# Kernel tuning notes

Hardware: AMD Instinct MI355X
Metric: run time of the kernel (lower is better)

Reference implementation:

```python
import jax, jax.numpy as jnp
import numpy as np

N, E = 50000, 800000
D_IN, D_DEG, D_H, D_UP = 96, 32, 256, 128
EPS = 0.0  # non-trainable buffer, initial_eps=0


def setup_inputs() -> dict:
    key = jax.random.key(0)
    ks = jax.random.split(key, 8)
    d = D_IN + D_DEG  # 128, feature dim after degree-as-tag concat
    return {
        "x": jax.random.normal(ks[0], (N, D_IN), dtype=jnp.float32),
        "degrees": jax.random.uniform(ks[1], (N, D_DEG), dtype=jnp.float32),
        "edge_features": jax.random.normal(ks[2], (E, d), dtype=jnp.float32),
        "W1": jax.random.normal(ks[3], (d, D_H), dtype=jnp.float32) * (1.0 / np.sqrt(d)),
        "b1": jnp.zeros((D_H,), dtype=jnp.float32),
        "W2": jax.random.normal(ks[4], (D_H, D_UP), dtype=jnp.float32) * (1.0 / np.sqrt(D_H)),
        "b2": jnp.zeros((D_UP,), dtype=jnp.float32),
        "edge_index": jax.random.randint(ks[5], (2, E), 0, N, dtype=jnp.int64),
    }


def reference(x, degrees, edge_features, W1, b1, W2, b2, edge_index):
    # degree_as_tag + retain_features: concat node features with degree tags
    h = jnp.concatenate([x, degrees], axis=-1)  # [N, 128]
    # flow='source_to_target': source j = edge_index[0], target i = edge_index[1]
    src, dst = edge_index[0], edge_index[1]
    msgs = jax.nn.relu(h[src] + edge_features)  # [E, 128]
    agg = jax.ops.segment_sum(msgs, dst, num_segments=N)  # [N, 128]
    z = (1.0 + EPS) * h + agg
    # update MLP: Linear -> ReLU -> Linear
    out = jax.nn.relu(z @ W1 + b1) @ W2 + b2  # [N, 128]
    return out
```

## Files before the change

### kernel.cpp

```cpp
#include <hip/hip_runtime.h>


constexpr int DIN  = 96;
constexpr int DDEG = 32;
constexpr int D    = 128;
constexpr int DH   = 256;
constexpr int DUP  = 128;

typedef short bf16x8 __attribute__((ext_vector_type(8)));
typedef float f32x4  __attribute__((ext_vector_type(4)));

static __device__ __forceinline__ ushort f2bf(float f) {
    unsigned u = __float_as_uint(f);
    unsigned r = (u + 0x7fff + ((u >> 16) & 1)) >> 16;
    return (ushort)r;
}
static __device__ __forceinline__ float4 bf4_to_f4(ushort4 u) {
    float4 r;
    r.x = __uint_as_float((unsigned)u.x << 16);
    r.y = __uint_as_float((unsigned)u.y << 16);
    r.z = __uint_as_float((unsigned)u.z << 16);
    r.w = __uint_as_float((unsigned)u.w << 16);
    return r;
}

static __device__ __forceinline__ int waveInclScan(int v, int lane) {
#pragma unroll
    for (int off = 1; off < 64; off <<= 1) {
        int t = __shfl_up(v, off, 64);
        if (lane >= off) v += t;
    }
    return v;
}

__global__ __launch_bounds__(256) void init_h_kernel(
    const float* __restrict__ x, const float* __restrict__ deg,
    ushort* __restrict__ hp, int N) {
    int t = blockIdx.x * 256 + threadIdx.x;
    if (t >= N * 32) return;
    int n = t >> 5, c = t & 31;
    float4 v;
    if (c < 24) v = *reinterpret_cast<const float4*>(&x[(size_t)n * DIN + c * 4]);
    else        v = *reinterpret_cast<const float4*>(&deg[(size_t)n * DDEG + (c - 24) * 4]);
    ushort4 o;
    o.x = f2bf(v.x); o.y = f2bf(v.y); o.z = f2bf(v.z); o.w = f2bf(v.w);
    *reinterpret_cast<ushort4*>(&hp[(size_t)n * D + c * 4]) = o;
}

__global__ __launch_bounds__(256) void count_kernel(
    const int* __restrict__ ei, int* __restrict__ counts, int N, int E) {
    int e = blockIdx.x * 256 + threadIdx.x;
    if (e >= E) return;
    atomicAdd(&counts[ei[E + e]], 1);
}

__global__ __launch_bounds__(256) void scan_partial_kernel(
    const int* __restrict__ counts, int* __restrict__ blockSums, int N) {
    const int tid = threadIdx.x;
    int base = blockIdx.x * 1024 + tid * 4;
    int4 c = make_int4(0, 0, 0, 0);
    if (base + 3 < N) c = *reinterpret_cast<const int4*>(&counts[base]);
    else if (base < N) {
        c.x = counts[base];
        if (base + 1 < N) c.y = counts[base + 1];
        if (base + 2 < N) c.z = counts[base + 2];
    }
    int s = c.x + c.y + c.z + c.w;
#pragma unroll
    for (int off = 32; off; off >>= 1) s += __shfl_xor(s, off, 64);
    __shared__ int wsum[4];
    if ((tid & 63) == 0) wsum[tid >> 6] = s;
    __syncthreads();
    if (tid == 0) blockSums[blockIdx.x] = wsum[0] + wsum[1] + wsum[2] + wsum[3];
}

__global__ __launch_bounds__(64) void scan_base_kernel(
    const int* __restrict__ blockSums, int* __restrict__ blockBase, int nb) {
    int l = threadIdx.x;
    int orig = (l < nb) ? blockSums[l] : 0;
    int incl = waveInclScan(orig, l);
    if (l < nb) blockBase[l] = incl - orig;
}

__global__ __launch_bounds__(256) void scan_final_kernel(
    const int* __restrict__ counts, const int* __restrict__ blockBase,
    int* __restrict__ offsets, int* __restrict__ cursor, int N, int E) {
    const int tid = threadIdx.x, lane = tid & 63, wave = tid >> 6;
    int base = blockIdx.x * 1024 + tid * 4;
    int4 c = make_int4(0, 0, 0, 0);
    if (base + 3 < N) c = *reinterpret_cast<const int4*>(&counts[base]);
    else if (base < N) {
        c.x = counts[base];
        if (base + 1 < N) c.y = counts[base + 1];
        if (base + 2 < N) c.z = counts[base + 2];
    }
    int s = c.x + c.y + c.z + c.w;
    int incl = waveInclScan(s, lane);
    __shared__ int wsum[4];
    if (lane == 63) wsum[wave] = incl;
    __syncthreads();
    int wb = 0;
#pragma unroll
    for (int w = 0; w < 4; ++w)
        if (w < wave) wb += wsum[w];
    int ex = blockBase[blockIdx.x] + wb + (incl - s);
    if (base < N)     { offsets[base]     = ex; cursor[base]     = ex; } ex += c.x;
    if (base + 1 < N) { offsets[base + 1] = ex; cursor[base + 1] = ex; } ex += c.y;
    if (base + 2 < N) { offsets[base + 2] = ex; cursor[base + 2] = ex; } ex += c.z;
    if (base + 3 < N) { offsets[base + 3] = ex; cursor[base + 3] = ex; }
    if (blockIdx.x == 0 && tid == 0) offsets[N] = E;
}

__global__ __launch_bounds__(256) void fill_kernel(
    const int* __restrict__ ei, int* __restrict__ cursor,
    int2* __restrict__ eids2, int E) {
    int e = blockIdx.x * 256 + threadIdx.x;
    if (e >= E) return;
    int src = ei[e];
    int dst = ei[E + e];
    int pos = atomicAdd(&cursor[dst], 1);
    eids2[pos] = make_int2(e, src);
}

__global__ __launch_bounds__(256) void gather_kernel(
    const ushort* __restrict__ hp, const float* __restrict__ ef,
    const int* __restrict__ offsets, const int2* __restrict__ eids2,
    ushort* __restrict__ zb, int N) {
    const int wave = threadIdx.x >> 6, lane = threadIdx.x & 63;
    const int node = blockIdx.x * 4 + wave;
    if (node >= N) return;
    const int c = lane & 31;
    const int eh = lane >> 5;

    float4 h = bf4_to_f4(*reinterpret_cast<const ushort4*>(&hp[(size_t)node * D + c * 4]));

    float4 acc = make_float4(0.f, 0.f, 0.f, 0.f);
    const int pBeg = offsets[node], pEnd = offsets[node + 1];
    int p = pBeg + eh;
    for (; p + 2 < pEnd; p += 4) {
        int2 ea = eids2[p];
        int2 eb = eids2[p + 2];
        f32x4 f0 = __builtin_nontemporal_load(
            reinterpret_cast<const f32x4*>(&ef[(size_t)ea.x * D + c * 4]));
        f32x4 f1 = __builtin_nontemporal_load(
            reinterpret_cast<const f32x4*>(&ef[(size_t)eb.x * D + c * 4]));
        float4 h0 = bf4_to_f4(*reinterpret_cast<const ushort4*>(&hp[(size_t)ea.y * D + c * 4]));
        float4 h1 = bf4_to_f4(*reinterpret_cast<const ushort4*>(&hp[(size_t)eb.y * D + c * 4]));
        acc.x += fmaxf(f0[0] + h0.x, 0.f) + fmaxf(f1[0] + h1.x, 0.f);
        acc.y += fmaxf(f0[1] + h0.y, 0.f) + fmaxf(f1[1] + h1.y, 0.f);
        acc.z += fmaxf(f0[2] + h0.z, 0.f) + fmaxf(f1[2] + h1.z, 0.f);
        acc.w += fmaxf(f0[3] + h0.w, 0.f) + fmaxf(f1[3] + h1.w, 0.f);
    }
    for (; p < pEnd; p += 2) {
        int2 ea = eids2[p];
        f32x4 f0 = __builtin_nontemporal_load(
            reinterpret_cast<const f32x4*>(&ef[(size_t)ea.x * D + c * 4]));
        float4 h0 = bf4_to_f4(*reinterpret_cast<const ushort4*>(&hp[(size_t)ea.y * D + c * 4]));
        acc.x += fmaxf(f0[0] + h0.x, 0.f);
        acc.y += fmaxf(f0[1] + h0.y, 0.f);
        acc.z += fmaxf(f0[2] + h0.z, 0.f);
        acc.w += fmaxf(f0[3] + h0.w, 0.f);
    }
    acc.x += __shfl_xor(acc.x, 32, 64);
    acc.y += __shfl_xor(acc.y, 32, 64);
    acc.z += __shfl_xor(acc.z, 32, 64);
    acc.w += __shfl_xor(acc.w, 32, 64);
    if (eh == 0) {
        ushort4 o;
        o.x = f2bf(h.x + acc.x);
        o.y = f2bf(h.y + acc.y);
        o.z = f2bf(h.z + acc.z);
        o.w = f2bf(h.w + acc.w);
        *reinterpret_cast<ushort4*>(&zb[(size_t)node * D + c * 4]) = o;
    }
}

__global__ __launch_bounds__(256) void pack_w_kernel(
    const float* __restrict__ W1, const float* __restrict__ W2,
    ushort* __restrict__ w1p, ushort* __restrict__ w2p) {
    int idx = blockIdx.x * 256 + threadIdx.x;
    if (idx >= 32768) return;
    {
        int j = idx & 7, l = (idx >> 3) & 63, nb = (idx >> 9) & 15, kb = idx >> 13;
        int k = kb * 32 + (l >> 4) * 8 + j, n = nb * 16 + (l & 15);
        w1p[idx] = f2bf(W1[k * DH + n]);
    }
    {
        int j = idx & 7, l = (idx >> 3) & 63, nb = (idx >> 9) & 7, kb = idx >> 12;
        int k = kb * 32 + (l >> 4) * 8 + j, n = nb * 16 + (l & 15);
        w2p[idx] = f2bf(W2[k * DUP + n]);
    }
}

__global__ __launch_bounds__(256) void mlp_mfma_kernel(
    const ushort* __restrict__ zb,
    const ushort* __restrict__ w1p, const float* __restrict__ b1,
    const ushort* __restrict__ w2p, const float* __restrict__ b2,
    float* __restrict__ out, int N) {
    __shared__ ushort u_lds[4][16][DH + 8];
    const int tid = threadIdx.x;
    const int wave = tid >> 6, lane = tid & 63;
    const int m0 = blockIdx.x * 64 + wave * 16;
    const int lr = lane & 15, lg = lane >> 4;

    bf16x8 a1[4];
    int rowA = m0 + lr; if (rowA > N - 1) rowA = N - 1;
    const ushort* zrow = &zb[(size_t)rowA * D + lg * 8];
#pragma unroll
    for (int kb = 0; kb < 4; ++kb)
        a1[kb] = *reinterpret_cast<const bf16x8*>(zrow + kb * 32);

#pragma unroll
    for (int nb = 0; nb < 16; ++nb) {
        f32x4 c = {0.f, 0.f, 0.f, 0.f};
#pragma unroll
        for (int kb = 0; kb < 4; ++kb) {
            bf16x8 b = *reinterpret_cast<const bf16x8*>(&w1p[((kb * 16 + nb) * 64 + lane) * 8]);
            c = __builtin_amdgcn_mfma_f32_16x16x32_bf16(a1[kb], b, c, 0, 0, 0);
        }
        float bias = b1[nb * 16 + lr];
#pragma unroll
        for (int r = 0; r < 4; ++r) {
            float v = fmaxf(c[r] + bias, 0.f);
            u_lds[wave][lg * 4 + r][nb * 16 + lr] = f2bf(v);
        }
    }
    __syncthreads();

    bf16x8 a2[8];
#pragma unroll
    for (int kb = 0; kb < 8; ++kb)
        a2[kb] = *reinterpret_cast<const bf16x8*>(&u_lds[wave][lr][kb * 32 + lg * 8]);

#pragma unroll
    for (int nb = 0; nb < 8; ++nb) {
        f32x4 c = {0.f, 0.f, 0.f, 0.f};
#pragma unroll
        for (int kb = 0; kb < 8; ++kb) {
            bf16x8 b = *reinterpret_cast<const bf16x8*>(&w2p[((kb * 8 + nb) * 64 + lane) * 8]);
            c = __builtin_amdgcn_mfma_f32_16x16x32_bf16(a2[kb], b, c, 0, 0, 0);
        }
        float bias = b2[nb * 16 + lr];
#pragma unroll
        for (int r = 0; r < 4; ++r) {
            int row = m0 + lg * 4 + r;
            if (row < N) out[(size_t)row * DUP + nb * 16 + lr] = c[r] + bias;
        }
    }
}

extern "C" void kernel_launch(void* const* d_in, const int* in_sizes, int n_in,
                              void* d_out, int out_size, void* d_ws, size_t ws_size,
                              hipStream_t stream) {
    const float* x   = (const float*)d_in[0];
    const float* dg  = (const float*)d_in[1];
    const float* ef  = (const float*)d_in[2];
    const float* W1  = (const float*)d_in[3];
    const float* b1  = (const float*)d_in[4];
    const float* W2  = (const float*)d_in[5];
    const float* b2  = (const float*)d_in[6];
    const int*   ei  = (const int*)d_in[7];
    float* out = (float*)d_out;

    const int N = in_sizes[0] / DIN;
    const int E = in_sizes[7] / 2;

    auto align16 = [](size_t v) { return (v + 15) & ~(size_t)15; };
    char* w = (char*)d_ws;
    ushort* zb      = (ushort*)w;  w += align16((size_t)N * D * 2);
    ushort* hp      = (ushort*)w;  w += align16((size_t)N * D * 2);
    int*   counts   = (int*)w;     w += align16((size_t)N * 4);
    int*   offsets  = (int*)w;     w += align16((size_t)(N + 1) * 4);
    int*   cursor   = (int*)w;     w += align16((size_t)N * 4);
    int2*  eids2    = (int2*)w;    w += align16((size_t)E * 8);
    int*   blockSums= (int*)w;     w += align16(64 * 4);
    int*   blockBase= (int*)w;     w += align16(64 * 4);
    ushort* w1p     = (ushort*)w;  w += align16((size_t)D * DH * 2);
    ushort* w2p     = (ushort*)w;  w += align16((size_t)DH * DUP * 2);

    hipMemsetAsync(counts, 0, (size_t)N * 4, stream);

    const int eb = (E + 255) / 256;
    const int nbScan = (N + 1023) / 1024;

    init_h_kernel<<<(N * 32 + 255) / 256, 256, 0, stream>>>(x, dg, hp, N);
    count_kernel<<<eb, 256, 0, stream>>>(ei, counts, N, E);
    scan_partial_kernel<<<nbScan, 256, 0, stream>>>(counts, blockSums, N);
    scan_base_kernel<<<1, 64, 0, stream>>>(blockSums, blockBase, nbScan);
    scan_final_kernel<<<nbScan, 256, 0, stream>>>(counts, blockBase, offsets, cursor, N, E);
    fill_kernel<<<eb, 256, 0, stream>>>(ei, cursor, eids2, E);

    gather_kernel<<<(N + 3) / 4, 256, 0, stream>>>(hp, ef, offsets, eids2, zb, N);

    pack_w_kernel<<<128, 256, 0, stream>>>(W1, W2, w1p, w2p);
    mlp_mfma_kernel<<<(N + 63) / 64, 256, 0, stream>>>(zb, w1p, b1, w2p, b2, out, N);
}
```

Before: 249.2 us.

## Assign one half-wave per node in gather and fold counts memset into init

The gather kernel now maps 32 lanes to each node (8 nodes per block) instead of a full 64-lane wave that split edges across two halves. Each half-wave walks its node's edge list alone with a 4-way unrolled loop, which removes the cross-half shuffle reduction and the idle half-wave on low-degree nodes. Separately, zeroing the degree counts moves into init_h_kernel, dropping the hipMemsetAsync call. Per-node serial edge work doubles, which may lengthen the tail for high-degree nodes.

Result: faster. 242.7 us (-2.6%).

```diff
diff --git a/kernel.cpp b/kernel.cpp
--- a/kernel.cpp
+++ b/kernel.cpp
@@ -35,8 +35,12 @@
 
 __global__ __launch_bounds__(256) void init_h_kernel(
     const float* __restrict__ x, const float* __restrict__ deg,
-    ushort* __restrict__ hp, int N) {
+    ushort* __restrict__ hp, int* __restrict__ counts, int N) {
     int t = blockIdx.x * 256 + threadIdx.x;
+    if (t < (N >> 2)) *reinterpret_cast<int4*>(&counts[t * 4]) = make_int4(0, 0, 0, 0);
+    if (t == (N >> 2) && (N & 3)) {
+        for (int i = (N & ~3); i < N; ++i) counts[i] = 0;
+    }
     if (t >= N * 32) return;
     int n = t >> 5, c = t & 31;
     float4 v;
@@ -126,53 +130,58 @@
     const ushort* __restrict__ hp, const float* __restrict__ ef,
     const int* __restrict__ offsets, const int2* __restrict__ eids2,
     ushort* __restrict__ zb, int N) {
-    const int wave = threadIdx.x >> 6, lane = threadIdx.x & 63;
-    const int node = blockIdx.x * 4 + wave;
+    const int node = blockIdx.x * 8 + (threadIdx.x >> 5);
     if (node >= N) return;
-    const int c = lane & 31;
-    const int eh = lane >> 5;
+    const int c = threadIdx.x & 31;
 
     float4 h = bf4_to_f4(*reinterpret_cast<const ushort4*>(&hp[(size_t)node * D + c * 4]));
 
     float4 acc = make_float4(0.f, 0.f, 0.f, 0.f);
-    const int pBeg = offsets[node], pEnd = offsets[node + 1];
-    int p = pBeg + eh;
-    for (; p + 2 < pEnd; p += 4) {
-        int2 ea = eids2[p];
-        int2 eb = eids2[p + 2];
+    const int pEnd = offsets[node + 1];
+    int p = offsets[node];
+
+    for (; p + 4 <= pEnd; p += 4) {
+        int2 i0 = eids2[p + 0];
+        int2 i1 = eids2[p + 1];
+        int2 i2 = eids2[p + 2];
+        int2 i3 = eids2[p + 3];
         f32x4 f0 = __builtin_nontemporal_load(
-            reinterpret_cast<const f32x4*>(&ef[(size_t)ea.x * D + c * 4]));
+            reinterpret_cast<const f32x4*>(&ef[(size_t)i0.x * D + c * 4]));
         f32x4 f1 = __builtin_nontemporal_load(
-            reinterpret_cast<const f32x4*>(&ef[(size_t)eb.x * D + c * 4]));
-        float4 h0 = bf4_to_f4(*reinterpret_cast<const ushort4*>(&hp[(size_t)ea.y * D + c * 4]));
-        float4 h1 = bf4_to_f4(*reinterpret_cast<const ushort4*>(&hp[(size_t)eb.y * D + c * 4]));
-        acc.x += fmaxf(f0[0] + h0.x, 0.f) + fmaxf(f1[0] + h1.x, 0.f);
-        acc.y += fmaxf(f0[1] + h0.y, 0.f) + fmaxf(f1[1] + h1.y, 0.f);
-        acc.z += fmaxf(f0[2] + h0.z, 0.f) + fmaxf(f1[2] + h1.z, 0.f);
-        acc.w += fmaxf(f0[3] + h0.w, 0.f) + fmaxf(f1[3] + h1.w, 0.f);
-    }
-    for (; p < pEnd; p += 2) {
-        int2 ea = eids2[p];
+            reinterpret_cast<const f32x4*>(&ef[(size_t)i1.x * D + c * 4]));
+        f32x4 f2 = __builtin_nontemporal_load(
+            reinterpret_cast<const f32x4*>(&ef[(size_t)i2.x * D + c * 4]));
+        f32x4 f3 = __builtin_nontemporal_load(
+            reinterpret_cast<const f32x4*>(&ef[(size_t)i3.x * D + c * 4]));
+        float4 h0 = bf4_to_f4(*reinterpret_cast<const ushort4*>(&hp[(size_t)i0.y * D + c * 4]));
+        float4 h1 = bf4_to_f4(*reinterpret_cast<const ushort4*>(&hp[(size_t)i1.y * D + c * 4]));
+        float4 h2 = bf4_to_f4(*reinterpret_cast<const ushort4*>(&hp[(size_t)i2.y * D + c * 4]));
+        float4 h3 = bf4_to_f4(*reinterpret_cast<const ushort4*>(&hp[(size_t)i3.y * D + c * 4]));
+        acc.x += fmaxf(f0[0] + h0.x, 0.f) + fmaxf(f1[0] + h1.x, 0.f)
+               + fmaxf(f2[0] + h2.x, 0.f) + fmaxf(f3[0] + h3.x, 0.f);
+        acc.y += fmaxf(f0[1] + h0.y, 0.f) + fmaxf(f1[1] + h1.y, 0.f)
+               + fmaxf(f2[1] + h2.y, 0.f) + fmaxf(f3[1] + h3.y, 0.f);
+        acc.z += fmaxf(f0[2] + h0.z, 0.f) + fmaxf(f1[2] + h1.z, 0.f)
+               + fmaxf(f2[2] + h2.z, 0.f) + fmaxf(f3[2] + h3.z, 0.f);
+        acc.w += fmaxf(f0[3] + h0.w, 0.f) + fmaxf(f1[3] + h1.w, 0.f)
+               + fmaxf(f2[3] + h2.w, 0.f) + fmaxf(f3[3] + h3.w, 0.f);
+    }
+    for (; p < pEnd; ++p) {
+        int2 i0 = eids2[p];
         f32x4 f0 = __builtin_nontemporal_load(
-            reinterpret_cast<const f32x4*>(&ef[(size_t)ea.x * D + c * 4]));
-        float4 h0 = bf4_to_f4(*reinterpret_cast<const ushort4*>(&hp[(size_t)ea.y * D + c * 4]));
+            reinterpret_cast<const f32x4*>(&ef[(size_t)i0.x * D + c * 4]));
+        float4 h0 = bf4_to_f4(*reinterpret_cast<const ushort4*>(&hp[(size_t)i0.y * D + c * 4]));
         acc.x += fmaxf(f0[0] + h0.x, 0.f);
         acc.y += fmaxf(f0[1] + h0.y, 0.f);
         acc.z += fmaxf(f0[2] + h0.z, 0.f);
         acc.w += fmaxf(f0[3] + h0.w, 0.f);
     }
-    acc.x += __shfl_xor(acc.x, 32, 64);
-    acc.y += __shfl_xor(acc.y, 32, 64);
-    acc.z += __shfl_xor(acc.z, 32, 64);
-    acc.w += __shfl_xor(acc.w, 32, 64);
-    if (eh == 0) {
-        ushort4 o;
-        o.x = f2bf(h.x + acc.x);
-        o.y = f2bf(h.y + acc.y);
-        o.z = f2bf(h.z + acc.z);
-        o.w = f2bf(h.w + acc.w);
-        *reinterpret_cast<ushort4*>(&zb[(size_t)node * D + c * 4]) = o;
-    }
+    ushort4 o;
+    o.x = f2bf(h.x + acc.x);
+    o.y = f2bf(h.y + acc.y);
+    o.z = f2bf(h.z + acc.z);
+    o.w = f2bf(h.w + acc.w);
+    *reinterpret_cast<ushort4*>(&zb[(size_t)node * D + c * 4]) = o;
 }
 
 __global__ __launch_bounds__(256) void pack_w_kernel(
@@ -278,19 +287,17 @@
     ushort* w1p     = (ushort*)w;  w += align16((size_t)D * DH * 2);
     ushort* w2p     = (ushort*)w;  w += align16((size_t)DH * DUP * 2);
 
-    hipMemsetAsync(counts, 0, (size_t)N * 4, stream);
-
     const int eb = (E + 255) / 256;
     const int nbScan = (N + 1023) / 1024;
 
-    init_h_kernel<<<(N * 32 + 255) / 256, 256, 0, stream>>>(x, dg, hp, N);
+    init_h_kernel<<<(N * 32 + 255) / 256, 256, 0, stream>>>(x, dg, hp, counts, N);
     count_kernel<<<eb, 256, 0, stream>>>(ei, counts, N, E);
     scan_partial_kernel<<<nbScan, 256, 0, stream>>>(counts, blockSums, N);
     scan_base_kernel<<<1, 64, 0, stream>>>(blockSums, blockBase, nbScan);
     scan_final_kernel<<<nbScan, 256, 0, stream>>>(counts, blockBase, offsets, cursor, N, E);
     fill_kernel<<<eb, 256, 0, stream>>>(ei, cursor, eids2, E);
 
-    gather_kernel<<<(N + 3) / 4, 256, 0, stream>>>(hp, ef, offsets, eids2, zb, N);
+    gather_kernel<<<(N + 7) / 8, 256, 0, stream>>>(hp, ef, offsets, eids2, zb, N);
 
     pack_w_kernel<<<128, 256, 0, stream>>>(W1, W2, w1p, w2p);
     mlp_mfma_kernel<<<(N + 63) / 64, 256, 0, stream>>>(zb, w1p, b1, w2p, b2, out, N);
```
